# Performance work log

Hardware: AMD Instinct MI355X
Metric: run time of the kernel (lower is better)

## Reference

```python
import jax, jax.numpy as jnp
import numpy as np

N_NODES = 100000
N_RELS = 3
N_EDGES = 300000


def setup_inputs() -> dict:
    key = jax.random.key(0)
    ks = jax.random.split(key, 6)
    x = jax.random.normal(ks[0], (N_NODES, 128), dtype=jnp.float32)
    W1 = jax.random.normal(ks[1], (N_RELS, 128, 128), dtype=jnp.float32) * (128 ** -0.5)
    b1 = jnp.zeros((N_RELS, 128), dtype=jnp.float32)
    W2 = jax.random.normal(ks[2], (N_RELS, 128, 64), dtype=jnp.float32) * (128 ** -0.5)
    b2 = jnp.zeros((N_RELS, 64), dtype=jnp.float32)
    edges = jax.random.randint(ks[3], (N_RELS, 2, N_EDGES), 0, N_NODES, dtype=jnp.int64)
    return {"x": x, "W1": W1, "b1": b1, "W2": W2, "b2": b2, "edges": edges}


def _hetero_graphconv_layer(x, W, b, edges, n_nodes):
    """Sum over relations of GraphConv(norm='both'):
    y_r = D_in^{-1/2} A_r (D_out^{-1/2} x) W_r + b_r   (degrees clamped to >=1, DGL default).
    HeteroGraphConv default aggregate is 'sum'."""
    out = jnp.zeros((n_nodes, W.shape[-1]), dtype=x.dtype)
    ones = jnp.ones((edges.shape[-1],), dtype=x.dtype)
    for r in range(edges.shape[0]):  # small fixed loop over relation types
        src, dst = edges[r, 0], edges[r, 1]
        out_deg = jnp.clip(jax.ops.segment_sum(ones, src, num_segments=n_nodes), 1.0)
        in_deg = jnp.clip(jax.ops.segment_sum(ones, dst, num_segments=n_nodes), 1.0)
        # transform scaled source features, then sparse aggregate to destinations
        m = (x * (out_deg ** -0.5)[:, None]) @ W[r]          # [N, out_f]
        agg = jax.ops.segment_sum(m[src], dst, num_segments=n_nodes)  # SpMM via gather+scatter
        out = out + agg * (in_deg ** -0.5)[:, None] + b[r]
    return out


def reference(x, W1, b1, W2, b2, edges):
    n = x.shape[0]
    h = jax.nn.relu(_hetero_graphconv_layer(x, W1, b1, edges, n))
    h = jax.nn.relu(_hetero_graphconv_layer(h, W2, b2, edges, n))
    return h
```

## Files before the change

kernel.cpp:

```cpp
#include <hip/hip_runtime.h>
#include <hip/hip_bf16.h>
#include <stdint.h>


constexpr int TPB = 256;

typedef __attribute__((ext_vector_type(8))) short short8;
typedef __attribute__((ext_vector_type(4))) float f32x4;

__device__ __forceinline__ float bf2f(unsigned short u) {
    return __uint_as_float(((unsigned)u) << 16);
}
__device__ __forceinline__ unsigned short f2bf(float f) {
    return __bfloat16_as_ushort(__float2bfloat16(f));
}


__global__ void count_kernel(const int* __restrict__ edges, unsigned* __restrict__ cnt,
                             int total, int E, int N) {
    int i = blockIdx.x * blockDim.x + threadIdx.x;
    if (i >= total) return;
    atomicAdd(&cnt[(size_t)(i / E) * N + edges[i]], 1u);
}

__global__ __launch_bounds__(256) void scan_local_kernel(const unsigned* __restrict__ cnt,
                                                         int* __restrict__ off,
                                                         unsigned* __restrict__ bsum,
                                                         int N, int nb) {
    int r = blockIdx.x / nb, blk = blockIdx.x - r * nb;
    const unsigned* in = cnt + (size_t)(2 * r + 1) * N;
    int* o = off + (size_t)r * (N + 1);
    const int t = threadIdx.x, lane = t & 63, wid = t >> 6;
    int base = blk * 1024 + t * 4;
    unsigned v0 = (base + 0 < N) ? in[base + 0] : 0u;
    unsigned v1 = (base + 1 < N) ? in[base + 1] : 0u;
    unsigned v2 = (base + 2 < N) ? in[base + 2] : 0u;
    unsigned v3 = (base + 3 < N) ? in[base + 3] : 0u;
    unsigned p1 = v0, p2 = p1 + v1, p3 = p2 + v2, tt = p3 + v3;
    unsigned x = tt;
#pragma unroll
    for (int d = 1; d < 64; d <<= 1) {
        unsigned tmp = __shfl_up(x, d, 64);
        if (lane >= d) x += tmp;
    }
    __shared__ unsigned ws4[4];
    if (lane == 63) ws4[wid] = x;
    __syncthreads();
    unsigned woff = 0;
#pragma unroll
    for (int w2 = 0; w2 < 4; ++w2)
        if (w2 < wid) woff += ws4[w2];
    unsigned excl = woff + x - tt;
    if (base + 0 < N) o[base + 0] = (int)excl;
    if (base + 1 < N) o[base + 1] = (int)(excl + p1);
    if (base + 2 < N) o[base + 2] = (int)(excl + p2);
    if (base + 3 < N) o[base + 3] = (int)(excl + p3);
    if (t == 255) bsum[r * nb + blk] = woff + x;
}

__global__ __launch_bounds__(128) void scan_bsum_kernel(unsigned* __restrict__ bsum,
                                                        int* __restrict__ off,
                                                        int nb, int N, int E) {
    const int t = threadIdx.x, lane = t & 63, wid = t >> 6;
    __shared__ unsigned wtot[2];
    for (int r = 0; r < 3; ++r) {
        unsigned v = (t < nb) ? bsum[r * nb + t] : 0u;
        unsigned x = v;
#pragma unroll
        for (int d = 1; d < 64; d <<= 1) {
            unsigned tmp = __shfl_up(x, d, 64);
            if (lane >= d) x += tmp;
        }
        if (lane == 63) wtot[wid] = x;
        __syncthreads();
        unsigned add = (wid == 1) ? wtot[0] : 0u;
        if (t < nb) bsum[r * nb + t] = add + x - v;
        if (t == 0) off[(size_t)r * (N + 1) + N] = E;
        __syncthreads();
    }
}

__global__ void finalize_off_kernel(int* __restrict__ off, const unsigned* __restrict__ bsum,
                                    int* __restrict__ cur, int N, int nb) {
    int i = blockIdx.x * blockDim.x + threadIdx.x;
    if (i >= 3 * N) return;
    int r = i / N, n = i - r * N;
    int v = off[(size_t)r * (N + 1) + n] + (int)bsum[r * nb + (n >> 10)];
    off[(size_t)r * (N + 1) + n] = v;
    cur[i] = v;
}

__global__ void fill_kernel(const int* __restrict__ edges, int* __restrict__ cur,
                            int* __restrict__ csr_src, int E, int N) {
    int gid = blockIdx.x * blockDim.x + threadIdx.x;
    if (gid >= 3 * E) return;
    int r = gid / E, e = gid - r * E;
    int d  = edges[(size_t)(2 * r + 1) * E + e];
    int sv = edges[(size_t)(2 * r) * E + e];
    int pos = atomicAdd(&cur[(size_t)r * N + d], 1);
    csr_src[(size_t)r * E + pos] = sv;
}

__global__ void scale_inplace_kernel(unsigned* __restrict__ buf, int total) {
    int i = blockIdx.x * blockDim.x + threadIdx.x;
    if (i >= total) return;
    unsigned c = buf[i];
    ((float*)buf)[i] = rsqrtf((float)(c ? c : 1u));
}


template <int CH, typename XT>
__global__ __launch_bounds__(256) void mfma_gemm3_kernel(const XT* __restrict__ X,
                                                         const float* __restrict__ W,
                                                         int WS, int c0,
                                                         __hip_bfloat16* __restrict__ T, int N) {
    constexpr int CT = CH / 16;
    constexpr int FR = 4 * CT;
    __shared__ short bs[3 * FR * 512];
    const int t = threadIdx.x;
    const int lane = t & 63, wv = t >> 6;
    const int m0 = blockIdx.x * 64;

    constexpr int TOT = 3 * 32 * CH;
    for (int linear = t; linear < TOT; linear += 256) {
        int rrel = linear / (32 * CH);
        int rem = linear - rrel * (32 * CH);
        int r4 = rem / CH, cc = rem - r4 * CH;
        int r = r4 << 2;
        const float* wp = W + (size_t)rrel * 128 * WS + (size_t)r * WS + c0 + cc;
        unsigned u0 = f2bf(wp[0]);
        unsigned u1 = f2bf(wp[WS]);
        unsigned u2 = f2bf(wp[2 * WS]);
        unsigned u3 = f2bf(wp[3 * WS]);
        int kk = r4 >> 3, jg = (r4 >> 1) & 3, j0 = (r4 & 1) * 4;
        int l = jg * 16 + (cc & 15), c = cc >> 4;
        int slot = ((rrel * FR + kk * CT + c) << 9) + l * 8 + j0;
        *reinterpret_cast<uint2*>(&bs[slot]) = make_uint2(u0 | (u1 << 16), u2 | (u3 << 16));
    }

    const int row = m0 + wv * 16 + (lane & 15);
    const bool ok = row < N;
    short8 a[4];
    if constexpr (sizeof(XT) == 4) {
        const float* xr = (const float*)X + (size_t)row * 128 + ((lane >> 4) << 3);
#pragma unroll
        for (int kk = 0; kk < 4; ++kk) {
            short8 av = {};
            if (ok) {
                float4 f0 = *reinterpret_cast<const float4*>(xr + kk * 32);
                float4 f1 = *reinterpret_cast<const float4*>(xr + kk * 32 + 4);
                av[0] = (short)f2bf(f0.x); av[1] = (short)f2bf(f0.y);
                av[2] = (short)f2bf(f0.z); av[3] = (short)f2bf(f0.w);
                av[4] = (short)f2bf(f1.x); av[5] = (short)f2bf(f1.y);
                av[6] = (short)f2bf(f1.z); av[7] = (short)f2bf(f1.w);
            }
            a[kk] = av;
        }
    } else {
        const short* xr = (const short*)X + (size_t)row * 128 + ((lane >> 4) << 3);
#pragma unroll
        for (int kk = 0; kk < 4; ++kk) {
            short8 av = {};
            if (ok) av = *reinterpret_cast<const short8*>(xr + kk * 32);
            a[kk] = av;
        }
    }

    __syncthreads();

    f32x4 acc4[3 * CT];
#pragma unroll
    for (int f = 0; f < 3 * CT; ++f) acc4[f] = {0.f, 0.f, 0.f, 0.f};
#pragma unroll
    for (int rrel = 0; rrel < 3; ++rrel) {
#pragma unroll
        for (int c = 0; c < CT; ++c) {
#pragma unroll
            for (int kk = 0; kk < 4; ++kk) {
                short8 b = *reinterpret_cast<const short8*>(
                    &bs[((rrel * FR + kk * CT + c) << 9) + lane * 8]);
                acc4[rrel * CT + c] =
                    __builtin_amdgcn_mfma_f32_16x16x32_bf16(a[kk], b, acc4[rrel * CT + c], 0, 0, 0);
            }
        }
    }

#pragma unroll
    for (int rrel = 0; rrel < 3; ++rrel) {
        __hip_bfloat16* Tr = T + (size_t)rrel * N * CH;
#pragma unroll
        for (int c = 0; c < CT; ++c) {
            int gcol = c * 16 + (lane & 15);
            f32x4 v = acc4[rrel * CT + c];
#pragma unroll
            for (int q = 0; q < 4; ++q) {
                int grow = m0 + wv * 16 + ((lane >> 4) << 2) + q;
                if (grow < N) Tr[(size_t)grow * CH + gcol] = __float2bfloat16(v[q]);
            }
        }
    }
}


template <int CH, int PHASE>
__global__ __launch_bounds__(256) void gather3_kernel(const int* __restrict__ off,
                                                      const int* __restrict__ csr,
                                                      const __hip_bfloat16* __restrict__ T,
                                                      const float* __restrict__ s,
                                                      const float* __restrict__ b, int FT, int c0,
                                                      float* __restrict__ outp,
                                                      __hip_bfloat16* __restrict__ h,
                                                      int N, int E) {
    constexpr int LPN = CH / 4;
    int gid = blockIdx.x * blockDim.x + threadIdx.x;
    int n = gid / LPN;
    if (n >= N) return;
    int j = (gid % LPN) * 4;
    int bj = c0 + j;
    float ox = b[bj + 0] + b[FT + bj + 0] + b[2 * FT + bj + 0];
    float oy = b[bj + 1] + b[FT + bj + 1] + b[2 * FT + bj + 1];
    float oz = b[bj + 2] + b[FT + bj + 2] + b[2 * FT + bj + 2];
    float ow = b[bj + 3] + b[FT + bj + 3] + b[2 * FT + bj + 3];
#pragma unroll
    for (int r = 0; r < 3; ++r) {
        const int* offr = off + (size_t)r * (N + 1);
        const int* csrr = csr + (size_t)r * E;
        const float* s_out = s + (size_t)(2 * r) * N;
        const __hip_bfloat16* Tr = T + (size_t)r * N * CH;
        int e0 = offr[n], e1 = offr[n + 1];
        float sx = 0.f, sy = 0.f, sz = 0.f, sw = 0.f;
        for (int e = e0; e < e1; ++e) {
            int sN = csrr[e];
            float w = s_out[sN];
            ushort4 raw = *reinterpret_cast<const ushort4*>(&Tr[(size_t)sN * CH + j]);
            sx += w * bf2f(raw.x);
            sy += w * bf2f(raw.y);
            sz += w * bf2f(raw.z);
            sw += w * bf2f(raw.w);
        }
        float si = s[(size_t)(2 * r + 1) * N + n];
        ox += si * sx; oy += si * sy; oz += si * sz; ow += si * sw;
    }
    if constexpr (PHASE == 0) {
        ushort4 o;
        o.x = f2bf(fmaxf(ox, 0.f));
        o.y = f2bf(fmaxf(oy, 0.f));
        o.z = f2bf(fmaxf(oz, 0.f));
        o.w = f2bf(fmaxf(ow, 0.f));
        *reinterpret_cast<ushort4*>(&h[(size_t)n * 128 + c0 + j]) = o;
    } else {
        float4 o;
        o.x = fmaxf(ox, 0.f);
        o.y = fmaxf(oy, 0.f);
        o.z = fmaxf(oz, 0.f);
        o.w = fmaxf(ow, 0.f);
        *reinterpret_cast<float4*>(&outp[(size_t)n * 64 + c0 + j]) = o;
    }
}

static inline int cdiv(int a, int b) { return (a + b - 1) / b; }

template <int CH>
static void run_pipeline(const float* x, const float* W1, const float* b1,
                         const float* W2, const float* b2, const int* edges,
                         float* out, void* d_ws, int N, int E, hipStream_t stream) {
    const int nb = cdiv(N, 1024);
    auto align256 = [](char* p) { return (char*)(((uintptr_t)p + 255) & ~(uintptr_t)255); };
    char* w = (char*)d_ws;
    unsigned* cnt = (unsigned*)w;
    float* s = (float*)w;                       w = align256(w + (size_t)6 * N * 4);
    __hip_bfloat16* h = (__hip_bfloat16*)w;     w = align256(w + (size_t)N * 128 * 2);
    __hip_bfloat16* T = (__hip_bfloat16*)w;     w = align256(w + (size_t)3 * N * CH * 2);
    int* off = (int*)w;                         w = align256(w + (size_t)3 * (N + 1) * 4);
    int* csr = (int*)w;
    int* cur = (int*)T;
    unsigned* bsum = (unsigned*)((char*)T + (size_t)3 * N * 4 + 256);

    hipMemsetAsync(cnt, 0, (size_t)6 * N * 4, stream);
    count_kernel<<<cdiv(6 * E, TPB), TPB, 0, stream>>>(edges, cnt, 6 * E, E, N);
    scan_local_kernel<<<3 * nb, 256, 0, stream>>>(cnt, off, bsum, N, nb);
    scan_bsum_kernel<<<1, 128, 0, stream>>>(bsum, off, nb, N, E);
    finalize_off_kernel<<<cdiv(3 * N, TPB), TPB, 0, stream>>>(off, bsum, cur, N, nb);
    fill_kernel<<<cdiv(3 * E, TPB), TPB, 0, stream>>>(edges, cur, csr, E, N);
    scale_inplace_kernel<<<cdiv(6 * N, TPB), TPB, 0, stream>>>(cnt, 6 * N);

    const int mgrid = cdiv(N, 64);
    const int ggrid = cdiv(N * (CH / 4), TPB);

    for (int c0 = 0; c0 < 128; c0 += CH) {
        mfma_gemm3_kernel<CH, float><<<mgrid, 256, 0, stream>>>(x, W1, 128, c0, T, N);
        gather3_kernel<CH, 0><<<ggrid, TPB, 0, stream>>>(off, csr, T, s, b1, 128, c0,
                                                         nullptr, h, N, E);
    }
    for (int c0 = 0; c0 < 64; c0 += CH) {
        mfma_gemm3_kernel<CH, __hip_bfloat16><<<mgrid, 256, 0, stream>>>(h, W2, 64, c0, T, N);
        gather3_kernel<CH, 1><<<ggrid, TPB, 0, stream>>>(off, csr, T, s, b2, 64, c0,
                                                         out, nullptr, N, E);
    }
}

extern "C" void kernel_launch(void* const* d_in, const int* in_sizes, int n_in,
                              void* d_out, int out_size, void* d_ws, size_t ws_size,
                              hipStream_t stream) {
    const float* x  = (const float*)d_in[0];
    const float* W1 = (const float*)d_in[1];
    const float* b1 = (const float*)d_in[2];
    const float* W2 = (const float*)d_in[3];
    const float* b2 = (const float*)d_in[4];
    const int*   edges = (const int*)d_in[5];
    float* out = (float*)d_out;

    const int N = in_sizes[0] / 128;
    const int E = in_sizes[5] / 6;

    const size_t need64 = (size_t)6 * N * 4 + (size_t)N * 128 * 2 + (size_t)3 * N * 64 * 2 +
                          (size_t)3 * (N + 1) * 4 + (size_t)3 * E * 4 + 4096;
    if (ws_size >= need64)
        run_pipeline<64>(x, W1, b1, W2, b2, edges, out, d_ws, N, E, stream);
    else
        run_pipeline<32>(x, W1, b1, W2, b2, edges, out, d_ws, N, E, stream);
}
```

Before: 495.9 us.

## Fold out-degree scale into GEMM epilogue and widen gather to 8 bf16 per thread

The source-side out-degree normalisation is now applied in the GEMM epilogue before T is stored, so the gather no longer loads s_out per edge. The gather kernel now handles 8 channels per thread with 16-byte loads and processes edges in pairs for more memory-level parallelism. The h buffer is placed in d_out to save workspace, CH is fixed to 64 and the CH=32 fallback is dropped. Storing h in the output buffer works only because the layer-2 GEMM finishes reading h before the final gather overwrites out, and scaling before the bf16 rounding slightly changes numerics.

Measured after the change: 461.2 us. 7.0% less time.

```diff
diff --git a/kernel.cpp b/kernel.cpp
--- a/kernel.cpp
+++ b/kernel.cpp
@@ -113,6 +113,7 @@
 __global__ __launch_bounds__(256) void mfma_gemm3_kernel(const XT* __restrict__ X,
                                                          const float* __restrict__ W,
                                                          int WS, int c0,
+                                                         const float* __restrict__ s,
                                                          __hip_bfloat16* __restrict__ T, int N) {
     constexpr int CT = CH / 16;
     constexpr int FR = 4 * CT;
@@ -187,15 +188,18 @@
 
 #pragma unroll
     for (int rrel = 0; rrel < 3; ++rrel) {
+        const float* so = s + (size_t)(2 * rrel) * N;
         __hip_bfloat16* Tr = T + (size_t)rrel * N * CH;
 #pragma unroll
-        for (int c = 0; c < CT; ++c) {
-            int gcol = c * 16 + (lane & 15);
-            f32x4 v = acc4[rrel * CT + c];
-#pragma unroll
-            for (int q = 0; q < 4; ++q) {
-                int grow = m0 + wv * 16 + ((lane >> 4) << 2) + q;
-                if (grow < N) Tr[(size_t)grow * CH + gcol] = __float2bfloat16(v[q]);
+        for (int q = 0; q < 4; ++q) {
+            int grow = m0 + wv * 16 + ((lane >> 4) << 2) + q;
+            if (grow < N) {
+                float sc = so[grow];
+#pragma unroll
+                for (int c = 0; c < CT; ++c) {
+                    int gcol = c * 16 + (lane & 15);
+                    Tr[(size_t)grow * CH + gcol] = __float2bfloat16(acc4[rrel * CT + c][q] * sc);
+                }
             }
         }
     }
@@ -211,93 +215,61 @@
                                                       float* __restrict__ outp,
                                                       __hip_bfloat16* __restrict__ h,
                                                       int N, int E) {
-    constexpr int LPN = CH / 4;
     int gid = blockIdx.x * blockDim.x + threadIdx.x;
-    int n = gid / LPN;
+    int n = gid >> 3;
     if (n >= N) return;
-    int j = (gid % LPN) * 4;
+    int j = (gid & 7) << 3;
     int bj = c0 + j;
-    float ox = b[bj + 0] + b[FT + bj + 0] + b[2 * FT + bj + 0];
-    float oy = b[bj + 1] + b[FT + bj + 1] + b[2 * FT + bj + 1];
-    float oz = b[bj + 2] + b[FT + bj + 2] + b[2 * FT + bj + 2];
-    float ow = b[bj + 3] + b[FT + bj + 3] + b[2 * FT + bj + 3];
+    float o[8];
+#pragma unroll
+    for (int k = 0; k < 8; ++k)
+        o[k] = b[bj + k] + b[FT + bj + k] + b[2 * FT + bj + k];
 #pragma unroll
     for (int r = 0; r < 3; ++r) {
         const int* offr = off + (size_t)r * (N + 1);
         const int* csrr = csr + (size_t)r * E;
-        const float* s_out = s + (size_t)(2 * r) * N;
         const __hip_bfloat16* Tr = T + (size_t)r * N * CH;
         int e0 = offr[n], e1 = offr[n + 1];
-        float sx = 0.f, sy = 0.f, sz = 0.f, sw = 0.f;
-        for (int e = e0; e < e1; ++e) {
-            int sN = csrr[e];
-            float w = s_out[sN];
-            ushort4 raw = *reinterpret_cast<const ushort4*>(&Tr[(size_t)sN * CH + j]);
-            sx += w * bf2f(raw.x);
-            sy += w * bf2f(raw.y);
-            sz += w * bf2f(raw.z);
-            sw += w * bf2f(raw.w);
+        float acc[8];
+#pragma unroll
+        for (int k = 0; k < 8; ++k) acc[k] = 0.f;
+        int e = e0;
+        for (; e + 2 <= e1; e += 2) {
+            int p0 = csrr[e], p1 = csrr[e + 1];
+            short8 r0 = *reinterpret_cast<const short8*>(&Tr[(size_t)p0 * CH + j]);
+            short8 r1 = *reinterpret_cast<const short8*>(&Tr[(size_t)p1 * CH + j]);
+#pragma unroll
+            for (int k = 0; k < 8; ++k)
+                acc[k] += bf2f((unsigned short)r0[k]) + bf2f((unsigned short)r1[k]);
+        }
+        if (e < e1) {
+            int p0 = csrr[e];
+            short8 r0 = *reinterpret_cast<const short8*>(&Tr[(size_t)p0 * CH + j]);
+#pragma unroll
+            for (int k = 0; k < 8; ++k) acc[k] += bf2f((unsigned short)r0[k]);
         }
         float si = s[(size_t)(2 * r + 1) * N + n];
-        ox += si * sx; oy += si * sy; oz += si * sz; ow += si * sw;
+#pragma unroll
+        for (int k = 0; k < 8; ++k) o[k] += si * acc[k];
     }
     if constexpr (PHASE == 0) {
-        ushort4 o;
-        o.x = f2bf(fmaxf(ox, 0.f));
-        o.y = f2bf(fmaxf(oy, 0.f));
-        o.z = f2bf(fmaxf(oz, 0.f));
-        o.w = f2bf(fmaxf(ow, 0.f));
-        *reinterpret_cast<ushort4*>(&h[(size_t)n * 128 + c0 + j]) = o;
+        short8 pk;
+#pragma unroll
+        for (int k = 0; k < 8; ++k) pk[k] = (short)f2bf(fmaxf(o[k], 0.f));
+        *reinterpret_cast<short8*>(&h[(size_t)n * 128 + c0 + j]) = pk;
     } else {
-        float4 o;
-        o.x = fmaxf(ox, 0.f);
-        o.y = fmaxf(oy, 0.f);
-        o.z = fmaxf(oz, 0.f);
-        o.w = fmaxf(ow, 0.f);
-        *reinterpret_cast<float4*>(&outp[(size_t)n * 64 + c0 + j]) = o;
+        float4 v0, v1;
+        v0.x = fmaxf(o[0], 0.f); v0.y = fmaxf(o[1], 0.f);
+        v0.z = fmaxf(o[2], 0.f); v0.w = fmaxf(o[3], 0.f);
+        v1.x = fmaxf(o[4], 0.f); v1.y = fmaxf(o[5], 0.f);
+        v1.z = fmaxf(o[6], 0.f); v1.w = fmaxf(o[7], 0.f);
+        float* p = &outp[(size_t)n * 64 + j];
+        *reinterpret_cast<float4*>(p) = v0;
+        *reinterpret_cast<float4*>(p + 4) = v1;
     }
 }
 
 static inline int cdiv(int a, int b) { return (a + b - 1) / b; }
-
-template <int CH>
-static void run_pipeline(const float* x, const float* W1, const float* b1,
-                         const float* W2, const float* b2, const int* edges,
-                         float* out, void* d_ws, int N, int E, hipStream_t stream) {
-    const int nb = cdiv(N, 1024);
-    auto align256 = [](char* p) { return (char*)(((uintptr_t)p + 255) & ~(uintptr_t)255); };
-    char* w = (char*)d_ws;
-    unsigned* cnt = (unsigned*)w;
-    float* s = (float*)w;                       w = align256(w + (size_t)6 * N * 4);
-    __hip_bfloat16* h = (__hip_bfloat16*)w;     w = align256(w + (size_t)N * 128 * 2);
-    __hip_bfloat16* T = (__hip_bfloat16*)w;     w = align256(w + (size_t)3 * N * CH * 2);
-    int* off = (int*)w;                         w = align256(w + (size_t)3 * (N + 1) * 4);
-    int* csr = (int*)w;
-    int* cur = (int*)T;
-    unsigned* bsum = (unsigned*)((char*)T + (size_t)3 * N * 4 + 256);
-
-    hipMemsetAsync(cnt, 0, (size_t)6 * N * 4, stream);
-    count_kernel<<<cdiv(6 * E, TPB), TPB, 0, stream>>>(edges, cnt, 6 * E, E, N);
-    scan_local_kernel<<<3 * nb, 256, 0, stream>>>(cnt, off, bsum, N, nb);
-    scan_bsum_kernel<<<1, 128, 0, stream>>>(bsum, off, nb, N, E);
-    finalize_off_kernel<<<cdiv(3 * N, TPB), TPB, 0, stream>>>(off, bsum, cur, N, nb);
-    fill_kernel<<<cdiv(3 * E, TPB), TPB, 0, stream>>>(edges, cur, csr, E, N);
-    scale_inplace_kernel<<<cdiv(6 * N, TPB), TPB, 0, stream>>>(cnt, 6 * N);
-
-    const int mgrid = cdiv(N, 64);
-    const int ggrid = cdiv(N * (CH / 4), TPB);
-
-    for (int c0 = 0; c0 < 128; c0 += CH) {
-        mfma_gemm3_kernel<CH, float><<<mgrid, 256, 0, stream>>>(x, W1, 128, c0, T, N);
-        gather3_kernel<CH, 0><<<ggrid, TPB, 0, stream>>>(off, csr, T, s, b1, 128, c0,
-                                                         nullptr, h, N, E);
-    }
-    for (int c0 = 0; c0 < 64; c0 += CH) {
-        mfma_gemm3_kernel<CH, __hip_bfloat16><<<mgrid, 256, 0, stream>>>(h, W2, 64, c0, T, N);
-        gather3_kernel<CH, 1><<<ggrid, TPB, 0, stream>>>(off, csr, T, s, b2, 64, c0,
-                                                         out, nullptr, N, E);
-    }
-}
 
 extern "C" void kernel_launch(void* const* d_in, const int* in_sizes, int n_in,
                               void* d_out, int out_size, void* d_ws, size_t ws_size,
@@ -312,11 +284,37 @@
 
     const int N = in_sizes[0] / 128;
     const int E = in_sizes[5] / 6;
-
-    const size_t need64 = (size_t)6 * N * 4 + (size_t)N * 128 * 2 + (size_t)3 * N * 64 * 2 +
-                          (size_t)3 * (N + 1) * 4 + (size_t)3 * E * 4 + 4096;
-    if (ws_size >= need64)
-        run_pipeline<64>(x, W1, b1, W2, b2, edges, out, d_ws, N, E, stream);
-    else
-        run_pipeline<32>(x, W1, b1, W2, b2, edges, out, d_ws, N, E, stream);
-}
+    const int nb = cdiv(N, 1024);
+    constexpr int CH = 64;
+
+    auto align256 = [](char* p) { return (char*)(((uintptr_t)p + 255) & ~(uintptr_t)255); };
+    char* w = (char*)d_ws;
+    unsigned* cnt = (unsigned*)w;
+    float* s = (float*)w;                       w = align256(w + (size_t)6 * N * 4);
+    __hip_bfloat16* T = (__hip_bfloat16*)w;     w = align256(w + (size_t)3 * N * CH * 2);
+    int* off = (int*)w;                         w = align256(w + (size_t)3 * (N + 1) * 4);
+    int* csr = (int*)w;
+    int* cur = (int*)T;
+    unsigned* bsum = (unsigned*)((char*)T + (size_t)3 * N * 4 + 256);
+    __hip_bfloat16* h = (__hip_bfloat16*)d_out;
+
+    hipMemsetAsync(cnt, 0, (size_t)6 * N * 4, stream);
+    count_kernel<<<cdiv(6 * E, TPB), TPB, 0, stream>>>(edges, cnt, 6 * E, E, N);
+    scan_local_kernel<<<3 * nb, 256, 0, stream>>>(cnt, off, bsum, N, nb);
+    scan_bsum_kernel<<<1, 128, 0, stream>>>(bsum, off, nb, N, E);
+    finalize_off_kernel<<<cdiv(3 * N, TPB), TPB, 0, stream>>>(off, bsum, cur, N, nb);
+    fill_kernel<<<cdiv(3 * E, TPB), TPB, 0, stream>>>(edges, cur, csr, E, N);
+    scale_inplace_kernel<<<cdiv(6 * N, TPB), TPB, 0, stream>>>(cnt, 6 * N);
+
+    const int mgrid = cdiv(N, 64);
+    const int ggrid = cdiv(N * 8, TPB);
+
+    for (int c0 = 0; c0 < 128; c0 += CH) {
+        mfma_gemm3_kernel<CH, float><<<mgrid, 256, 0, stream>>>(x, W1, 128, c0, s, T, N);
+        gather3_kernel<CH, 0><<<ggrid, TPB, 0, stream>>>(off, csr, T, s, b1, 128, c0,
+                                                         nullptr, h, N, E);
+    }
+    mfma_gemm3_kernel<CH, __hip_bfloat16><<<mgrid, 256, 0, stream>>>(h, W2, 64, 0, s, T, N);
+    gather3_kernel<CH, 1><<<ggrid, TPB, 0, stream>>>(off, csr, T, s, b2, 64, 0,
+                                                     out, nullptr, N, E);
+}
```
